# Kernel tuning notes

Measured on AMD Instinct MI355X. Metric: run time of the kernel, lower is better.

## Reference

```python
import jax, jax.numpy as jnp
import numpy as np

B, S, HID = 2, 2048, 2048
H, D = 16, 128        # num_heads, kv_channels
LAYER_IDX = 4
MASK_VALUE = -10000.0


def setup_inputs() -> dict:
    key = jax.random.key(0)
    ks = jax.random.split(key, 5)
    hidden_states = jax.random.normal(ks[0], (B, S, HID), dtype=jnp.float32)
    # causal mask, broadcastable to [B, q, H, k] per torch.where(mask, w, mask_value)
    causal = jnp.tril(jnp.ones((S, S), dtype=bool))
    attention_mask = jnp.broadcast_to(causal[None, :, None, :], (B, S, 1, S))
    Wq = jax.random.normal(ks[1], (HID, H * D), dtype=jnp.float32) * (HID ** -0.5)
    bq = jnp.zeros((H * D,), dtype=jnp.float32)
    Wkv = jax.random.normal(ks[2], (HID, 2 * D), dtype=jnp.float32) * (HID ** -0.5)
    bkv = jnp.zeros((2 * D,), dtype=jnp.float32)
    Wp = jax.random.normal(ks[3], (H * D, HID), dtype=jnp.float32) * ((H * D) ** -0.5)
    bp = jnp.zeros((HID,), dtype=jnp.float32)
    return {"hidden_states": hidden_states, "attention_mask": attention_mask,
            "Wq": Wq, "bq": bq, "Wkv": Wkv, "bkv": bkv, "Wp": Wp, "bp": bp}


def reference(hidden_states, attention_mask, Wq, bq, Wkv, bkv, Wp, bp):
    # projections
    q = hidden_states @ Wq + bq                      # [B,S,H*D]
    kv = hidden_states @ Wkv + bkv                   # [B,S,2D]
    k, v = kv[..., :D], kv[..., D:]                  # shared single K/V head [B,S,D]
    qh = q.reshape(B, S, H, D)
    # baddbmm with alpha = 1/(layer_idx * sqrt(D))
    scale_factor = (1.0 / LAYER_IDX) / (D ** 0.5)
    scores = jnp.einsum('bqhd,bkd->bqhk', qh, k) * scale_factor  # [B,q,H,k]
    # upcast softmax with unscale = layer_idx, masked with -1e4
    scores = scores.astype(jnp.float32) * LAYER_IDX
    scores = jnp.where(attention_mask, scores, MASK_VALUE)
    weights = jax.nn.softmax(scores, axis=-1).astype(hidden_states.dtype)
    attn = jnp.einsum('bqhk,bkd->bqhd', weights, v).reshape(B, S, H * D)
    out = attn @ Wp + bp
    return out
```

## Files before the change

### kernel.cpp

```cpp
#include <hip/hip_runtime.h>

#define DEVI __device__ __forceinline__

typedef unsigned int u32;
typedef unsigned short u16;

constexpr int Bc = 2, Sc = 2048, HIDc = 2048, Hc = 16, Dc = 128;
constexpr int Mrows = Bc * Sc;
constexpr float SCALE = 0.08838834764831845f;
constexpr float M0 = 16.0f;

typedef float f32x4 __attribute__((ext_vector_type(4)));
typedef __bf16 bf16x8 __attribute__((ext_vector_type(8)));

DEVI float bf2f(u16 v) { return __builtin_bit_cast(float, (u32)v << 16); }
DEVI u16 f2bf(float x) {
  u32 u = __builtin_bit_cast(u32, x);
  u32 r = (u + 0x7fffu + ((u >> 16) & 1u)) >> 16;
  return (u16)r;
}

DEVI void async16(void* lds, const void* g) {
  __builtin_amdgcn_global_load_lds((const __attribute__((address_space(1))) void*)g,
                                   (__attribute__((address_space(3))) void*)lds,
                                   16, 0, 0);
}

constexpr int PRE_BLOCKS = 6289;
constexpr int TS = 66;

DEVI void do_transpose64(const void* in, u16* out, int R, int C, int c0, int r0, bool bf,
                         u16* tile, int tid) {
  const int cg = (tid & 7) * 8, ry = tid >> 3;
#pragma unroll
  for (int p = 0; p < 2; ++p) {
    int r = ry + p * 32;
    size_t idx = (size_t)(r0 + r) * C + (c0 + cg);
    u16 tmp[8];
    if (bf) {
      *(uint4*)tmp = *(const uint4*)&((const u16*)in)[idx];
    } else {
      const float* f = (const float*)in + idx;
#pragma unroll
      for (int j = 0; j < 8; ++j) tmp[j] = f2bf(f[j]);
    }
    *(uint4*)&tile[r * TS + cg] = *(const uint4*)tmp;
  }
  __syncthreads();
  const int rx = (tid & 7) * 8, cy = tid >> 3;
#pragma unroll
  for (int p = 0; p < 2; ++p) {
    int c = cy + p * 32;
    u16 tmp[8];
#pragma unroll
    for (int j = 0; j < 8; ++j) tmp[j] = tile[(rx + j) * TS + c];
    *(uint4*)&out[(size_t)(c0 + c) * R + r0 + rx] = *(const uint4*)tmp;
  }
}

__global__ __launch_bounds__(256) void pre_kernel(const void* __restrict__ hs,
                                                  const void* __restrict__ Wq,
                                                  const void* __restrict__ bq,
                                                  const void* __restrict__ Wkv,
                                                  const void* __restrict__ bkv,
                                                  const void* __restrict__ Wp,
                                                  const void* __restrict__ bp,
                                                  u16* __restrict__ HSb, u16* __restrict__ WqT,
                                                  u16* __restrict__ WkvT, u16* __restrict__ WpT,
                                                  u16* __restrict__ biasB, int* __restrict__ flag) {
  __shared__ int cnt;
  __shared__ u16 tile[64 * TS];
  const int tid = threadIdx.x, bx = blockIdx.x;
  if (tid == 0) cnt = 0;
  __syncthreads();
  int ok = 0;
  const u32* hw = (const u32*)hs;
  for (int i = tid; i < 512; i += 256) {
    u32 lo = hw[i] & 0xffffu;
    u32 e = (lo >> 7) & 0xffu;
    if (lo == 0u || (e >= 118u && e <= 134u)) ok++;
  }
  atomicAdd(&cnt, ok);
  __syncthreads();
  const bool bf = cnt > 256;
  if (bx == 0 && tid == 0) *flag = bf ? 1 : 0;

  if (bx < 4096) {
    int i = (bx * 256 + tid) * 8;
    if (bf) {
      *(uint4*)&HSb[i] = *(const uint4*)&((const u16*)hs)[i];
    } else {
      const float* f = (const float*)hs;
      u16 tmp[8];
#pragma unroll
      for (int j = 0; j < 8; ++j) tmp[j] = f2bf(f[i + j]);
      *(uint4*)&HSb[i] = *(const uint4*)tmp;
    }
  } else if (bx < 5120) {
    int t = bx - 4096;
    do_transpose64(Wq, WqT, 2048, 2048, (t & 31) * 64, (t >> 5) * 64, bf, tile, tid);
  } else if (bx < 5248) {
    int t = bx - 5120;
    do_transpose64(Wkv, WkvT, 2048, 256, (t & 3) * 64, (t >> 2) * 64, bf, tile, tid);
  } else if (bx < 6272) {
    int t = bx - 5248;
    do_transpose64(Wp, WpT, 2048, 2048, (t & 31) * 64, (t >> 5) * 64, bf, tile, tid);
  } else {
    int i = (bx - 6272) * 256 + tid;
    if (i < 4352) {
      const void* src;
      int j;
      if (i < 2048) { src = bq; j = i; }
      else if (i < 2304) { src = bkv; j = i - 2048; }
      else { src = bp; j = i - 2304; }
      biasB[i] = bf ? ((const u16*)src)[j] : f2bf(((const float*)src)[j]);
    }
  }
}

__global__ __launch_bounds__(512, 4) void gemm_bt(const u16* __restrict__ A,
                                                  const u16* __restrict__ BT,
                                                  const u16* __restrict__ bias,
                                                  void* __restrict__ C,
                                                  int M, int N, int K,
                                                  const int* __restrict__ flag,
                                                  int mode) {
  __shared__ __align__(16) u16 As[2][128 * 32];
  __shared__ __align__(16) u16 Bs[2][128 * 32];
  const int tid = threadIdx.x;
  const int bm = blockIdx.x, bn = blockIdx.y;
  const int wave = tid >> 6, lane = tid & 63;
  const int wm = (wave & 3) * 32, wn = (wave >> 2) * 64;
  const int lr = lane & 15, kq = lane >> 4;
  f32x4 acc[2][4] = {};
  const size_t a_base = (size_t)bm * 128 * K;
  const size_t b_base = (size_t)bn * 128 * K;

#define STAGE(k0, buf)                                                             \
  {                                                                                \
    int r = tid >> 2, c = tid & 3;                                                 \
    int gc = (c ^ (r & 3)) << 3;                                                   \
    async16(&As[buf][tid * 8], A + a_base + (size_t)r * K + (k0) + gc);            \
    async16(&Bs[buf][tid * 8], BT + b_base + (size_t)r * K + (k0) + gc);           \
  }

  STAGE(0, 0);
  const int nsteps = K >> 5;
  for (int s = 0; s < nsteps; ++s) {
    const int cur = s & 1;
    asm volatile("s_waitcnt vmcnt(0)" ::: "memory");
    asm volatile("s_barrier" ::: "memory");
    if (s + 1 < nsteps) STAGE((s + 1) << 5, cur ^ 1);
    bf16x8 af[2], bfr[4];
#pragma unroll
    for (int i = 0; i < 2; ++i) {
      int ra = wm + i * 16 + lr;
      af[i] = *(const bf16x8*)&As[cur][ra * 32 + ((kq ^ (ra & 3)) << 3)];
    }
#pragma unroll
    for (int i = 0; i < 4; ++i) {
      int rb = wn + i * 16 + lr;
      bfr[i] = *(const bf16x8*)&Bs[cur][rb * 32 + ((kq ^ (rb & 3)) << 3)];
    }
#pragma unroll
    for (int mi = 0; mi < 2; ++mi)
#pragma unroll
      for (int ni = 0; ni < 4; ++ni)
        acc[mi][ni] = __builtin_amdgcn_mfma_f32_16x16x32_bf16(af[mi], bfr[ni], acc[mi][ni], 0, 0, 0);
  }
#undef STAGE

  if (mode == 3) {
    u16* Qout = (u16*)C;
    u16* KsG = Qout + (size_t)4096 * 2048;
    u16* VtG = KsG + (size_t)4096 * 128;
    const bool isQ = (bn < 16);
#pragma unroll
    for (int mi = 0; mi < 2; ++mi)
#pragma unroll
      for (int ni = 0; ni < 4; ++ni) {
        int col = bn * 128 + wn + ni * 16 + lr;
        float bv = bf2f(bias[col]);
#pragma unroll
        for (int rr = 0; rr < 4; ++rr) {
          int row = bm * 128 + wm + mi * 16 + kq * 4 + rr;
          u16 v = f2bf(acc[mi][ni][rr] + bv);
          if (isQ) {
            Qout[(size_t)row * 2048 + col] = v;
          } else {
            int c2 = col - 2048;
            if (c2 < 128) {
              int d = c2;
              KsG[(size_t)row * 128 + (((d >> 3) ^ (row & 15)) << 3) + (d & 7)] = v;
            } else {
              int d = c2 - 128, bb = row >> 11, s = row & 2047;
              VtG[((size_t)(bb * 128 + d)) * 2048 + (s & ~63) +
                  ((((s >> 3) & 7) ^ (d & 7)) << 3) + (s & 7)] = v;
            }
          }
        }
      }
    return;
  }
  const bool out16 = (mode == 0) || (*flag != 0);
#pragma unroll
  for (int mi = 0; mi < 2; ++mi)
#pragma unroll
    for (int ni = 0; ni < 4; ++ni) {
      int col = bn * 128 + wn + ni * 16 + lr;
      float bv = bf2f(bias[col]);
#pragma unroll
      for (int rr = 0; rr < 4; ++rr) {
        int row = bm * 128 + wm + mi * 16 + kq * 4 + rr;
        float v = acc[mi][ni][rr] + bv;
        size_t idx = (size_t)row * N + col;
        if (out16) ((u16*)C)[idx] = f2bf(v);
        else ((float*)C)[idx] = v;
      }
    }
}

constexpr int PS_STRIDE = 72;

__global__ __launch_bounds__(256) void flash_mfma(const u16* __restrict__ Q,
                                                  const u16* __restrict__ KsG,
                                                  const u16* __restrict__ VtG,
                                                  u16* __restrict__ O) {
  __shared__ __align__(16) u16 Ks[2][64 * 128];
  __shared__ __align__(16) u16 Vt[2][128 * 64];
  __shared__ __align__(16) u16 Ps[64 * PS_STRIDE];
  const int pairidx = blockIdx.x, h = blockIdx.y, b = blockIdx.z;
  const int tid = threadIdx.x;
  const int wave = tid >> 6, lane = tid & 63;
  const int lr = lane & 15, kq = lane >> 4;

  for (int half = 0; half < 2; ++half) {
    const int qt = (half == 0) ? pairidx : 31 - pairidx;
    bf16x8 qf[4];
    const u16* qbase = Q + ((size_t)(b * 2048 + qt * 64 + wave * 16 + lr)) * 2048 + h * 128;
#pragma unroll
    for (int kk = 0; kk < 4; ++kk)
      qf[kk] = *(const bf16x8*)(qbase + kk * 32 + kq * 8);
    f32x4 of[8] = {};
    float lsum[4] = {0.f, 0.f, 0.f, 0.f};
    const int srow = qt * 64 + wave * 16 + kq * 4;
    const int kmax = qt * 64;

    {
      const u16* g = KsG + ((size_t)(b * 2048)) * 128;
#pragma unroll
      for (int it = 0; it < 4; ++it)
        async16(&Ks[0][it * 2048 + tid * 8], g + it * 2048 + tid * 8);
      const size_t vbase = ((size_t)b * 128) * 2048;
#pragma unroll
      for (int it = 0; it < 4; ++it) {
        int chunk = it * 256 + tid;
        async16(&Vt[0][chunk * 8], VtG + vbase + (size_t)(chunk >> 3) * 2048 + (chunk & 7) * 8);
      }
    }

    for (int k0 = 0; k0 <= kmax; k0 += 64) {
      const int cur = (k0 >> 6) & 1;
      asm volatile("s_waitcnt vmcnt(0)" ::: "memory");
      asm volatile("s_barrier" ::: "memory");
      if (k0 + 64 <= kmax) {
        const int nxt = cur ^ 1;
        const u16* g = KsG + ((size_t)(b * 2048 + k0 + 64)) * 128;
#pragma unroll
        for (int it = 0; it < 4; ++it)
          async16(&Ks[nxt][it * 2048 + tid * 8], g + it * 2048 + tid * 8);
        const size_t vbase = ((size_t)b * 128) * 2048 + k0 + 64;
#pragma unroll
        for (int it = 0; it < 4; ++it) {
          int chunk = it * 256 + tid;
          async16(&Vt[nxt][chunk * 8], VtG + vbase + (size_t)(chunk >> 3) * 2048 + (chunk & 7) * 8);
        }
      }

      const bool diag = (k0 == kmax);
      f32x4 sf[4] = {};
#pragma unroll
      for (int nt = 0; nt < 4; ++nt) {
        int keyl = nt * 16 + lr;
#pragma unroll
        for (int kk = 0; kk < 4; ++kk) {
          const bf16x8 kf = *(const bf16x8*)&Ks[cur][keyl * 128 + ((((kk << 2) + kq) ^ lr) << 3)];
          sf[nt] = __builtin_amdgcn_mfma_f32_16x16x32_bf16(qf[kk], kf, sf[nt], 0, 0, 0);
        }
      }
#pragma unroll
      for (int nt = 0; nt < 4; ++nt) {
        int t = k0 + nt * 16 + lr;
#pragma unroll
        for (int r = 0; r < 4; ++r) {
          float v = fmaf(sf[nt][r], SCALE, -M0);
          if (diag && t > srow + r) v = -1e30f;
          float p = __expf(v);
          lsum[r] += p;
          Ps[(wave * 16 + kq * 4 + r) * PS_STRIDE + nt * 16 + lr] = f2bf(p);
        }
      }
#pragma unroll
      for (int ks = 0; ks < 2; ++ks) {
        const bf16x8 pf = *(const bf16x8*)&Ps[(wave * 16 + lr) * PS_STRIDE + ks * 32 + kq * 8];
#pragma unroll
        for (int dt = 0; dt < 8; ++dt) {
          int d = dt * 16 + lr;
          const bf16x8 vf = *(const bf16x8*)&Vt[cur][d * 64 + ((((ks << 2) + kq) ^ (d & 7)) << 3)];
          of[dt] = __builtin_amdgcn_mfma_f32_16x16x32_bf16(pf, vf, of[dt], 0, 0, 0);
        }
      }
    }
    float linv[4];
#pragma unroll
    for (int r = 0; r < 4; ++r) {
      float l = lsum[r];
      l += __shfl_xor(l, 1);
      l += __shfl_xor(l, 2);
      l += __shfl_xor(l, 4);
      l += __shfl_xor(l, 8);
      linv[r] = 1.f / l;
    }
    u16* obase = O + ((size_t)(b * 2048 + qt * 64 + wave * 16 + kq * 4)) * 2048 + h * 128;
#pragma unroll
    for (int dt = 0; dt < 8; ++dt)
#pragma unroll
      for (int r = 0; r < 4; ++r)
        obase[(size_t)r * 2048 + dt * 16 + lr] = f2bf(of[dt][r] * linv[r]);
    __syncthreads();
  }
}

extern "C" void kernel_launch(void* const* d_in, const int* in_sizes, int n_in,
                              void* d_out, int out_size, void* d_ws, size_t ws_size,
                              hipStream_t stream) {
  (void)in_sizes; (void)n_in; (void)out_size; (void)ws_size;
  const void* hs  = d_in[0];
  const void* Wq  = d_in[2];
  const void* bq  = d_in[3];
  const void* Wkv = d_in[4];
  const void* bkv = d_in[5];
  const void* Wp  = d_in[6];
  const void* bp  = d_in[7];

  char* ws = (char*)d_ws;
  int* flag  = (int*)(ws + 0);
  u16* HSb   = (u16*)(ws + 256);
  u16* WqT   = (u16*)(ws + 16777472);
  u16* WkvT  = (u16*)(ws + 25166080);
  u16* WpT   = (u16*)(ws + 26214656);
  u16* biasB = (u16*)(ws + 34603264);
  u16* Qb    = (u16*)(ws + 34611968);
  u16* KsG   = (u16*)(ws + 51389184);
  u16* VtG   = (u16*)(ws + 52437760);
  u16* ATTNb = (u16*)(ws + 53486336);

  pre_kernel<<<PRE_BLOCKS, 256, 0, stream>>>(hs, Wq, bq, Wkv, bkv, Wp, bp,
                                             HSb, WqT, WkvT, WpT, biasB, flag);
  gemm_bt<<<dim3(32, 18), 512, 0, stream>>>(HSb, WqT, biasB, Qb, 4096, 2304, 2048, flag, 3);
  flash_mfma<<<dim3(16, 16, 2), 256, 0, stream>>>(Qb, KsG, VtG, ATTNb);
  gemm_bt<<<dim3(32, 16), 512, 0, stream>>>(ATTNb, WpT, biasB + 2304, d_out, 4096, 2048, 2048, flag, 1);
}
```

Before: 308.7 us.

## Run both causal query tiles concurrently in flash block and skip bf16 input copy

The flash kernel now launches 512 threads per block, with two groups of four waves each processing one of the paired query tiles (early and late) at the same time over a shared K/V stream. Previously the two tiles were handled one after the other. The shorter tile's waves skip compute once past their causal limit but keep joining barriers and loads. P scratch moves to per-wave swizzled LDS buffers to reduce bank conflicts. When the input is already bf16, the hidden-state copy is dropped and the first GEMM reads the input directly via a flag-selected pointer.

After: 316.2 us. 1.02x slower.

```diff
diff --git a/kernel.cpp b/kernel.cpp
--- a/kernel.cpp
+++ b/kernel.cpp
@@ -86,16 +86,13 @@
   if (bx == 0 && tid == 0) *flag = bf ? 1 : 0;
 
   if (bx < 4096) {
+    if (bf) return;
     int i = (bx * 256 + tid) * 8;
-    if (bf) {
-      *(uint4*)&HSb[i] = *(const uint4*)&((const u16*)hs)[i];
-    } else {
-      const float* f = (const float*)hs;
-      u16 tmp[8];
-#pragma unroll
-      for (int j = 0; j < 8; ++j) tmp[j] = f2bf(f[i + j]);
-      *(uint4*)&HSb[i] = *(const uint4*)tmp;
-    }
+    const float* f = (const float*)hs;
+    u16 tmp[8];
+#pragma unroll
+    for (int j = 0; j < 8; ++j) tmp[j] = f2bf(f[i + j]);
+    *(uint4*)&HSb[i] = *(const uint4*)tmp;
   } else if (bx < 5120) {
     int t = bx - 4096;
     do_transpose64(Wq, WqT, 2048, 2048, (t & 31) * 64, (t >> 5) * 64, bf, tile, tid);
@@ -118,7 +115,8 @@
   }
 }
 
-__global__ __launch_bounds__(512, 4) void gemm_bt(const u16* __restrict__ A,
+__global__ __launch_bounds__(512, 4) void gemm_bt(const u16* __restrict__ A0,
+                                                  const u16* __restrict__ A1,
                                                   const u16* __restrict__ BT,
                                                   const u16* __restrict__ bias,
                                                   void* __restrict__ C,
@@ -127,6 +125,7 @@
                                                   int mode) {
   __shared__ __align__(16) u16 As[2][128 * 32];
   __shared__ __align__(16) u16 Bs[2][128 * 32];
+  const u16* __restrict__ A = (*flag != 0) ? A1 : A0;
   const int tid = threadIdx.x;
   const int bm = blockIdx.x, bn = blockIdx.y;
   const int wave = tid >> 6, lane = tid & 63;
@@ -220,115 +219,114 @@
     }
 }
 
-constexpr int PS_STRIDE = 72;
-
-__global__ __launch_bounds__(256) void flash_mfma(const u16* __restrict__ Q,
-                                                  const u16* __restrict__ KsG,
-                                                  const u16* __restrict__ VtG,
-                                                  u16* __restrict__ O) {
+__global__ __launch_bounds__(512, 4) void flash_mfma(const u16* __restrict__ Q,
+                                                     const u16* __restrict__ KsG,
+                                                     const u16* __restrict__ VtG,
+                                                     u16* __restrict__ O) {
   __shared__ __align__(16) u16 Ks[2][64 * 128];
   __shared__ __align__(16) u16 Vt[2][128 * 64];
-  __shared__ __align__(16) u16 Ps[64 * PS_STRIDE];
+  __shared__ __align__(16) u16 Ps[8][16 * 64];
   const int pairidx = blockIdx.x, h = blockIdx.y, b = blockIdx.z;
   const int tid = threadIdx.x;
   const int wave = tid >> 6, lane = tid & 63;
   const int lr = lane & 15, kq = lane >> 4;
-
-  for (int half = 0; half < 2; ++half) {
-    const int qt = (half == 0) ? pairidx : 31 - pairidx;
-    bf16x8 qf[4];
-    const u16* qbase = Q + ((size_t)(b * 2048 + qt * 64 + wave * 16 + lr)) * 2048 + h * 128;
-#pragma unroll
-    for (int kk = 0; kk < 4; ++kk)
-      qf[kk] = *(const bf16x8*)(qbase + kk * 32 + kq * 8);
-    f32x4 of[8] = {};
-    float lsum[4] = {0.f, 0.f, 0.f, 0.f};
-    const int srow = qt * 64 + wave * 16 + kq * 4;
-    const int kmax = qt * 64;
-
-    {
-      const u16* g = KsG + ((size_t)(b * 2048)) * 128;
-#pragma unroll
-      for (int it = 0; it < 4; ++it)
-        async16(&Ks[0][it * 2048 + tid * 8], g + it * 2048 + tid * 8);
-      const size_t vbase = ((size_t)b * 128) * 2048;
-#pragma unroll
-      for (int it = 0; it < 4; ++it) {
-        int chunk = it * 256 + tid;
-        async16(&Vt[0][chunk * 8], VtG + vbase + (size_t)(chunk >> 3) * 2048 + (chunk & 7) * 8);
-      }
-    }
-
-    for (int k0 = 0; k0 <= kmax; k0 += 64) {
-      const int cur = (k0 >> 6) & 1;
-      asm volatile("s_waitcnt vmcnt(0)" ::: "memory");
-      asm volatile("s_barrier" ::: "memory");
-      if (k0 + 64 <= kmax) {
-        const int nxt = cur ^ 1;
-        const u16* g = KsG + ((size_t)(b * 2048 + k0 + 64)) * 128;
-#pragma unroll
-        for (int it = 0; it < 4; ++it)
-          async16(&Ks[nxt][it * 2048 + tid * 8], g + it * 2048 + tid * 8);
-        const size_t vbase = ((size_t)b * 128) * 2048 + k0 + 64;
-#pragma unroll
-        for (int it = 0; it < 4; ++it) {
-          int chunk = it * 256 + tid;
-          async16(&Vt[nxt][chunk * 8], VtG + vbase + (size_t)(chunk >> 3) * 2048 + (chunk & 7) * 8);
-        }
-      }
-
-      const bool diag = (k0 == kmax);
-      f32x4 sf[4] = {};
-#pragma unroll
-      for (int nt = 0; nt < 4; ++nt) {
-        int keyl = nt * 16 + lr;
-#pragma unroll
-        for (int kk = 0; kk < 4; ++kk) {
-          const bf16x8 kf = *(const bf16x8*)&Ks[cur][keyl * 128 + ((((kk << 2) + kq) ^ lr) << 3)];
-          sf[nt] = __builtin_amdgcn_mfma_f32_16x16x32_bf16(qf[kk], kf, sf[nt], 0, 0, 0);
-        }
-      }
-#pragma unroll
-      for (int nt = 0; nt < 4; ++nt) {
-        int t = k0 + nt * 16 + lr;
-#pragma unroll
-        for (int r = 0; r < 4; ++r) {
-          float v = fmaf(sf[nt][r], SCALE, -M0);
-          if (diag && t > srow + r) v = -1e30f;
-          float p = __expf(v);
-          lsum[r] += p;
-          Ps[(wave * 16 + kq * 4 + r) * PS_STRIDE + nt * 16 + lr] = f2bf(p);
-        }
-      }
-#pragma unroll
-      for (int ks = 0; ks < 2; ++ks) {
-        const bf16x8 pf = *(const bf16x8*)&Ps[(wave * 16 + lr) * PS_STRIDE + ks * 32 + kq * 8];
-#pragma unroll
-        for (int dt = 0; dt < 8; ++dt) {
-          int d = dt * 16 + lr;
-          const bf16x8 vf = *(const bf16x8*)&Vt[cur][d * 64 + ((((ks << 2) + kq) ^ (d & 7)) << 3)];
-          of[dt] = __builtin_amdgcn_mfma_f32_16x16x32_bf16(pf, vf, of[dt], 0, 0, 0);
-        }
-      }
-    }
-    float linv[4];
-#pragma unroll
-    for (int r = 0; r < 4; ++r) {
-      float l = lsum[r];
-      l += __shfl_xor(l, 1);
-      l += __shfl_xor(l, 2);
-      l += __shfl_xor(l, 4);
-      l += __shfl_xor(l, 8);
-      linv[r] = 1.f / l;
-    }
-    u16* obase = O + ((size_t)(b * 2048 + qt * 64 + wave * 16 + kq * 4)) * 2048 + h * 128;
-#pragma unroll
-    for (int dt = 0; dt < 8; ++dt)
-#pragma unroll
-      for (int r = 0; r < 4; ++r)
-        obase[(size_t)r * 2048 + dt * 16 + lr] = f2bf(of[dt][r] * linv[r]);
-    __syncthreads();
-  }
+  const int qw = wave & 3, grp = wave >> 2;
+  const int qt = grp ? (31 - pairidx) : pairidx;
+  const int kmax = qt * 64;
+  const int kmaxblk = (31 - pairidx) * 64;
+
+  bf16x8 qf[4];
+  const u16* qbase = Q + ((size_t)(b * 2048 + qt * 64 + qw * 16 + lr)) * 2048 + h * 128;
+#pragma unroll
+  for (int kk = 0; kk < 4; ++kk)
+    qf[kk] = *(const bf16x8*)(qbase + kk * 32 + kq * 8);
+  f32x4 of[8] = {};
+  float lsum[4] = {0.f, 0.f, 0.f, 0.f};
+  const int srow = qt * 64 + qw * 16 + kq * 4;
+
+  {
+    const u16* g = KsG + ((size_t)(b * 2048)) * 128;
+#pragma unroll
+    for (int it = 0; it < 2; ++it)
+      async16(&Ks[0][(it * 512 + tid) * 8], g + (it * 512 + tid) * 8);
+    const size_t vbase = ((size_t)b * 128) * 2048;
+#pragma unroll
+    for (int it = 0; it < 2; ++it) {
+      int ch = it * 512 + tid;
+      async16(&Vt[0][ch * 8], VtG + vbase + (size_t)(ch >> 3) * 2048 + (ch & 7) * 8);
+    }
+  }
+
+  for (int k0 = 0; k0 <= kmaxblk; k0 += 64) {
+    const int cur = (k0 >> 6) & 1;
+    asm volatile("s_waitcnt vmcnt(0)" ::: "memory");
+    asm volatile("s_barrier" ::: "memory");
+    if (k0 + 64 <= kmaxblk) {
+      const int nxt = cur ^ 1;
+      const u16* g = KsG + ((size_t)(b * 2048 + k0 + 64)) * 128;
+#pragma unroll
+      for (int it = 0; it < 2; ++it)
+        async16(&Ks[nxt][(it * 512 + tid) * 8], g + (it * 512 + tid) * 8);
+      const size_t vbase = ((size_t)b * 128) * 2048 + k0 + 64;
+#pragma unroll
+      for (int it = 0; it < 2; ++it) {
+        int ch = it * 512 + tid;
+        async16(&Vt[nxt][ch * 8], VtG + vbase + (size_t)(ch >> 3) * 2048 + (ch & 7) * 8);
+      }
+    }
+    if (k0 > kmax) continue;
+
+    const bool diag = (k0 == kmax);
+    f32x4 sf[4] = {};
+#pragma unroll
+    for (int nt = 0; nt < 4; ++nt) {
+      int keyl = nt * 16 + lr;
+#pragma unroll
+      for (int kk = 0; kk < 4; ++kk) {
+        const bf16x8 kf = *(const bf16x8*)&Ks[cur][keyl * 128 + ((((kk << 2) + kq) ^ lr) << 3)];
+        sf[nt] = __builtin_amdgcn_mfma_f32_16x16x32_bf16(qf[kk], kf, sf[nt], 0, 0, 0);
+      }
+    }
+#pragma unroll
+    for (int nt = 0; nt < 4; ++nt) {
+      int t = k0 + nt * 16 + lr;
+#pragma unroll
+      for (int r = 0; r < 4; ++r) {
+        float v = fmaf(sf[nt][r], SCALE, -M0);
+        if (diag && t > srow + r) v = -1e30f;
+        float p = __expf(v);
+        lsum[r] += p;
+        int row = kq * 4 + r;
+        Ps[wave][row * 64 + (((nt * 2 + (lr >> 3)) ^ (row & 7)) << 3) + (lr & 7)] = f2bf(p);
+      }
+    }
+#pragma unroll
+    for (int ks = 0; ks < 2; ++ks) {
+      const bf16x8 pf = *(const bf16x8*)&Ps[wave][lr * 64 + ((((ks << 2) + kq) ^ (lr & 7)) << 3)];
+#pragma unroll
+      for (int dt = 0; dt < 8; ++dt) {
+        int d = dt * 16 + lr;
+        const bf16x8 vf = *(const bf16x8*)&Vt[cur][d * 64 + ((((ks << 2) + kq) ^ (d & 7)) << 3)];
+        of[dt] = __builtin_amdgcn_mfma_f32_16x16x32_bf16(pf, vf, of[dt], 0, 0, 0);
+      }
+    }
+  }
+  float linv[4];
+#pragma unroll
+  for (int r = 0; r < 4; ++r) {
+    float l = lsum[r];
+    l += __shfl_xor(l, 1);
+    l += __shfl_xor(l, 2);
+    l += __shfl_xor(l, 4);
+    l += __shfl_xor(l, 8);
+    linv[r] = 1.f / l;
+  }
+  u16* obase = O + ((size_t)(b * 2048 + qt * 64 + qw * 16 + kq * 4)) * 2048 + h * 128;
+#pragma unroll
+  for (int dt = 0; dt < 8; ++dt)
+#pragma unroll
+    for (int r = 0; r < 4; ++r)
+      obase[(size_t)r * 2048 + dt * 16 + lr] = f2bf(of[dt][r] * linv[r]);
 }
 
 extern "C" void kernel_launch(void* const* d_in, const int* in_sizes, int n_in,
@@ -357,7 +355,9 @@
 
   pre_kernel<<<PRE_BLOCKS, 256, 0, stream>>>(hs, Wq, bq, Wkv, bkv, Wp, bp,
                                              HSb, WqT, WkvT, WpT, biasB, flag);
-  gemm_bt<<<dim3(32, 18), 512, 0, stream>>>(HSb, WqT, biasB, Qb, 4096, 2304, 2048, flag, 3);
-  flash_mfma<<<dim3(16, 16, 2), 256, 0, stream>>>(Qb, KsG, VtG, ATTNb);
-  gemm_bt<<<dim3(32, 16), 512, 0, stream>>>(ATTNb, WpT, biasB + 2304, d_out, 4096, 2048, 2048, flag, 1);
-}
+  gemm_bt<<<dim3(32, 18), 512, 0, stream>>>(HSb, (const u16*)hs, WqT, biasB, Qb,
+                                            4096, 2304, 2048, flag, 3);
+  flash_mfma<<<dim3(16, 16, 2), 512, 0, stream>>>(Qb, KsG, VtG, ATTNb);
+  gemm_bt<<<dim3(32, 16), 512, 0, stream>>>(ATTNb, ATTNb, WpT, biasB + 2304, d_out,
+                                            4096, 2048, 2048, flag, 1);
+}
```
